# Optimization experiments

Measured on AMD Instinct MI355X. Metric: run time of the kernel, lower is better.

## Reference

```python
import jax, jax.numpy as jnp
import numpy as np

B, T, D_MODEL, D_HEAD = 8, 2048, 1024, 64


def setup_inputs() -> dict:
    key = jax.random.key(0)
    kx, kq, kk, kv = jax.random.split(key, 4)
    s = 1.0 / np.sqrt(D_MODEL)
    return {
        "x": jax.random.normal(kx, (B, T, D_MODEL), dtype=jnp.float32),
        "W_Q": jax.random.normal(kq, (D_MODEL, D_HEAD), dtype=jnp.float32) * s,
        "W_K": jax.random.normal(kk, (D_MODEL, D_HEAD), dtype=jnp.float32) * s,
        "W_V": jax.random.normal(kv, (D_MODEL, D_HEAD), dtype=jnp.float32) * s,
    }


def reference(x, W_Q, W_K, W_V):
    # x: [B, T, d_model]; projections -> [B, T, d_head]
    q = jnp.einsum("btd,dh->bth", x, W_Q)
    k = jnp.einsum("btd,dh->bth", x, W_K)
    v = jnp.einsum("btd,dh->bth", x, W_V)
    d_head = W_Q.shape[-1]
    scale = 1.0 / jnp.sqrt(jnp.asarray(d_head, dtype=x.dtype))
    # scores: [B, T, T], causal mask (lower-triangular kept)
    scores = jnp.einsum("bqh,bkh->bqk", q, k) * scale
    T_ = x.shape[1]
    causal = jnp.tril(jnp.ones((T_, T_), dtype=bool))
    scores = jnp.where(causal[None, :, :], scores, jnp.asarray(-jnp.inf, dtype=x.dtype))
    a = jax.nn.softmax(scores, axis=-1)
    # dropout omitted (eval mode / identity)
    out = jnp.einsum("bqk,bkh->bqh", a, v)
    return out
```

## Files before the change

### kernel.cpp

```cpp
#include <hip/hip_runtime.h>

#define TT   2048
#define DM   1024
#define DH   64
#define NB   8
#define BK   128
#define KST  72

typedef __attribute__((ext_vector_type(4))) float          f32x4;
typedef __attribute__((ext_vector_type(4))) int            i32x4;
typedef __attribute__((ext_vector_type(4))) unsigned short u16x4;
typedef __attribute__((ext_vector_type(8))) short          s16x8;

__device__ __forceinline__ unsigned short f2bf(float f) {
  unsigned int u = __float_as_uint(f);
  u += 0x7fffu + ((u >> 16) & 1u);
  return (unsigned short)(u >> 16);
}

#define MFMA(acc, a, b) \
  (acc) = __builtin_amdgcn_mfma_f32_16x16x32_bf16((a), (b), (acc), 0, 0, 0)

__device__ __forceinline__ void gload_lds16(const void* g, void* l) {
  __builtin_amdgcn_global_load_lds(
      (const __attribute__((address_space(1))) void*)g,
      (__attribute__((address_space(3))) void*)l, 16, 0, 0);
}

#define WS_WT    0u
#define WS_QK    393216u
#define WS_VT    4587520u
#define WS_OP    6684672u
#define WS_ML    24510464u

__global__ __launch_bounds__(256) void pack_w_kernel(
    const float* __restrict__ wq, const float* __restrict__ wk,
    const float* __restrict__ wv, unsigned short* __restrict__ wt) {
  int idx = blockIdx.x * 256 + threadIdx.x;
  if (idx >= 192 * DM) return;
  int n = idx >> 10;
  int k = idx & (DM - 1);
  const float* src = (n < 64) ? wq : ((n < 128) ? wk : wv);
  wt[(size_t)n * DM + k] = f2bf(src[(size_t)k * DH + (n & 63)]);
}

__global__ __launch_bounds__(256) void qkv_gemm_kernel(
    const float* __restrict__ x, const unsigned short* __restrict__ wt,
    unsigned short* __restrict__ qkvqk, unsigned short* __restrict__ vt) {
  __shared__ __align__(16) float          a_lds[32 * BK];
  __shared__ __align__(16) unsigned short b_lds[192 * BK];

  const int tid  = threadIdx.x;
  const int lane = tid & 63;
  const int w    = tid >> 6;
  const int ln   = lane & 15;
  const int quad = lane >> 4;
  const int mw   = w & 1;
  const int nw   = w >> 1;
  const int m0   = blockIdx.x * 32;
  const int n0   = nw * 96;
  const int lsw  = ln & 7;

  int agoff[4];
  #pragma unroll
  for (int i = 0; i < 4; ++i) {
    int s = i * 256 + w * 64 + lane;
    int m = s >> 5, cc = s & 31;
    agoff[i] = (m0 + m) * DM + ((cc ^ (m & 7)) << 2);
  }
  int bgoff[12];
  #pragma unroll
  for (int j = 0; j < 12; ++j) {
    int s = j * 256 + w * 64 + lane;
    int n = s >> 4, cc = s & 15;
    bgoff[j] = n * DM + ((cc ^ (n & 7)) << 3);
  }

  f32x4 acc[6];
  #pragma unroll
  for (int i = 0; i < 6; ++i) acc[i] = (f32x4){0.f, 0.f, 0.f, 0.f};
  union { s16x8 v; unsigned short h[8]; } ap;

  #pragma unroll
  for (int i = 0; i < 4; ++i)
    gload_lds16(x + agoff[i], (void*)(a_lds + (i * 256 + w * 64) * 4));
  #pragma unroll
  for (int j = 0; j < 12; ++j)
    gload_lds16(wt + bgoff[j], (void*)(b_lds + (j * 256 + w * 64) * 8));

  for (int k0 = 0; k0 < DM; k0 += BK) {
    __syncthreads();
    #pragma unroll
    for (int ks = 0; ks < BK; ks += 32) {
      const int m  = mw * 16 + ln;
      const int c0 = (ks >> 2) + 2 * quad;
      f32x4 v0 = *(const f32x4*)&a_lds[m * BK + ((c0 ^ lsw) << 2)];
      f32x4 v1 = *(const f32x4*)&a_lds[m * BK + (((c0 + 1) ^ lsw) << 2)];
      #pragma unroll
      for (int j = 0; j < 4; ++j) { ap.h[j] = f2bf(v0[j]); ap.h[4 + j] = f2bf(v1[j]); }
      s16x8 af = ap.v;
      const int cb = (ks >> 3) + quad;
      #pragma unroll
      for (int nt = 0; nt < 6; ++nt) {
        int n = n0 + nt * 16 + ln;
        s16x8 bf = *(const s16x8*)&b_lds[n * BK + ((cb ^ lsw) << 3)];
        MFMA(acc[nt], af, bf);
      }
    }
    __syncthreads();
    if (k0 + BK < DM) {
      const int kn = k0 + BK;
      #pragma unroll
      for (int i = 0; i < 4; ++i)
        gload_lds16(x + agoff[i] + kn, (void*)(a_lds + (i * 256 + w * 64) * 4));
      #pragma unroll
      for (int j = 0; j < 12; ++j)
        gload_lds16(wt + bgoff[j] + kn, (void*)(b_lds + (j * 256 + w * 64) * 8));
    }
  }

  const float QS = 0.18033688011112042f;
  const int mm0 = m0 + mw * 16;
  const int bz  = mm0 >> 11;
  const int tb  = (mm0 & 2047) + quad * 4;
  #pragma unroll
  for (int nt = 0; nt < 6; ++nt) {
    const int ncol = n0 + nt * 16 + ln;
    if (ncol < 128) {
      const float sc = (ncol < 64) ? QS : 1.0f;
      #pragma unroll
      for (int r = 0; r < 4; ++r) {
        int row = mm0 + quad * 4 + r;
        qkvqk[(size_t)row * 128 + ncol] = f2bf(acc[nt][r] * sc);
      }
    } else {
      int d = ncol - 128;
      u16x4 h;
      #pragma unroll
      for (int r = 0; r < 4; ++r) h[r] = f2bf(acc[nt][r]);
      *(u16x4*)(vt + ((size_t)bz * 64 + d) * TT + tb) = h;
    }
  }
}

__global__ __launch_bounds__(256) void attn_part_kernel(
    const unsigned short* __restrict__ qkvqk, const unsigned short* __restrict__ vt,
    unsigned short* __restrict__ opart, float* __restrict__ ml) {
  const int Ctab[16] = {0,1,3,6,10,15,21,28,36,45,55,66,78,91,105,120};
  const int f  = blockIdx.x;
  const int bz = f / 136;
  const int rw = f - bz * 136;
  int s = 0;
  #pragma unroll
  for (int t = 1; t < 16; ++t) if (rw >= Ctab[t]) s = t;
  const int c = rw - Ctab[s];
  const int qtA = 2 * s, qtB = 2 * s + 1;

  __shared__ __align__(16) unsigned short k_lds[128 * 64];
  __shared__ __align__(16) unsigned short v_lds[64 * 128];
  __shared__ __align__(16) unsigned short p_lds[64 * KST];

  const int tid  = threadIdx.x;
  const int w    = tid >> 6;
  const int lane = tid & 63;
  const int ln   = lane & 15;
  const int quad = lane >> 4;
  const int lsw  = ln & 7;
  const int bb   = bz * TT;
  const int kbase = c * 128;

  #pragma unroll
  for (int i = 0; i < 4; ++i) {
    int base = (i * 4 + w) * 64;
    int slot = base + lane;
    int row = slot >> 3, cc = slot & 7;
    gload_lds16(qkvqk + (size_t)(bb + kbase + row) * 128 + 64 + ((cc ^ (row & 7)) << 3),
                (void*)(k_lds + base * 8));
  }
  #pragma unroll
  for (int i = 0; i < 4; ++i) {
    int base = (i * 4 + w) * 64;
    int slot = base + lane;
    int d = slot >> 4, cc = slot & 15;
    gload_lds16(vt + ((size_t)bz * 64 + d) * TT + kbase + ((cc ^ (d & 7)) << 3),
                (void*)(v_lds + base * 8));
  }

  const unsigned short* qrowA = qkvqk + (size_t)(bb + qtA * 64 + w * 16 + ln) * 128;
  const unsigned short* qrowB = qrowA + 64 * 128;
  const s16x8 qfA0 = *(const s16x8*)(qrowA + quad * 8);
  const s16x8 qfA1 = *(const s16x8*)(qrowA + 32 + quad * 8);
  const s16x8 qfB0 = *(const s16x8*)(qrowB + quad * 8);
  const s16x8 qfB1 = *(const s16x8*)(qrowB + 32 + quad * 8);

  s16x8 ones;
  #pragma unroll
  for (int j = 0; j < 8; ++j) ones[j] = (short)0x3F80;

  f32x4 acc_oA[4], acc_oB[4], acc_lA, acc_lB;
  #pragma unroll
  for (int i = 0; i < 4; ++i) {
    acc_oA[i] = (f32x4){0.f, 0.f, 0.f, 0.f};
    acc_oB[i] = (f32x4){0.f, 0.f, 0.f, 0.f};
  }
  acc_lA = (f32x4){0.f, 0.f, 0.f, 0.f};
  acc_lB = (f32x4){0.f, 0.f, 0.f, 0.f};

  const int qgA = qtA * 64 + w * 16 + quad * 4;
  const int qgB = qgA + 64;
  __syncthreads();

  #pragma unroll
  for (int ct = 0; ct < 2; ++ct) {
    const int ktg = c * 2 + ct;
    const int kc0 = quad;
    const int kc1 = 4 + quad;

    if (ktg <= qtA) {
      const bool diag = (ktg == qtA);
      f32x4 acc_s[4];
      #pragma unroll
      for (int i = 0; i < 4; ++i) acc_s[i] = (f32x4){0.f, 0.f, 0.f, 0.f};
      #pragma unroll
      for (int ns = 0; ns < 4; ++ns) {
        const int krow = ct * 64 + ns * 16 + ln;
        s16x8 kf0 = *(const s16x8*)&k_lds[krow * 64 + ((kc0 ^ lsw) << 3)];
        s16x8 kf1 = *(const s16x8*)&k_lds[krow * 64 + ((kc1 ^ lsw) << 3)];
        MFMA(acc_s[ns], qfA0, kf0);
        MFMA(acc_s[ns], qfA1, kf1);
      }
      #pragma unroll
      for (int r = 0; r < 4; ++r) {
        const int qg = qgA + r;
        #pragma unroll
        for (int ns = 0; ns < 4; ++ns) {
          float sv = acc_s[ns][r];
          if (diag) {
            int kg = ktg * 64 + ns * 16 + ln;
            sv = (kg <= qg) ? sv : -1e30f;
          }
          p_lds[(w * 16 + quad * 4 + r) * KST + ns * 16 + ln] = f2bf(exp2f(sv));
        }
      }
      #pragma unroll
      for (int kk = 0; kk < 64; kk += 32) {
        s16x8 pf = *(const s16x8*)&p_lds[(w * 16 + ln) * KST + kk + quad * 8];
        MFMA(acc_lA, pf, ones);
        #pragma unroll
        for (int nt = 0; nt < 4; ++nt) {
          const int d  = nt * 16 + ln;
          const int sc = (ct * 8 + (kk >> 3) + quad) ^ lsw;
          s16x8 vf = *(const s16x8*)&v_lds[d * 128 + sc * 8];
          MFMA(acc_oA[nt], pf, vf);
        }
      }
      asm volatile("" ::: "memory");
    }

    {
      const bool diag = (ktg == qtB);
      f32x4 acc_s[4];
      #pragma unroll
      for (int i = 0; i < 4; ++i) acc_s[i] = (f32x4){0.f, 0.f, 0.f, 0.f};
      #pragma unroll
      for (int ns = 0; ns < 4; ++ns) {
        const int krow = ct * 64 + ns * 16 + ln;
        s16x8 kf0 = *(const s16x8*)&k_lds[krow * 64 + ((kc0 ^ lsw) << 3)];
        s16x8 kf1 = *(const s16x8*)&k_lds[krow * 64 + ((kc1 ^ lsw) << 3)];
        MFMA(acc_s[ns], qfB0, kf0);
        MFMA(acc_s[ns], qfB1, kf1);
      }
      #pragma unroll
      for (int r = 0; r < 4; ++r) {
        const int qg = qgB + r;
        #pragma unroll
        for (int ns = 0; ns < 4; ++ns) {
          float sv = acc_s[ns][r];
          if (diag) {
            int kg = ktg * 64 + ns * 16 + ln;
            sv = (kg <= qg) ? sv : -1e30f;
          }
          p_lds[(w * 16 + quad * 4 + r) * KST + ns * 16 + ln] = f2bf(exp2f(sv));
        }
      }
      #pragma unroll
      for (int kk = 0; kk < 64; kk += 32) {
        s16x8 pf = *(const s16x8*)&p_lds[(w * 16 + ln) * KST + kk + quad * 8];
        MFMA(acc_lB, pf, ones);
        #pragma unroll
        for (int nt = 0; nt < 4; ++nt) {
          const int d  = nt * 16 + ln;
          const int sc = (ct * 8 + (kk >> 3) + quad) ^ lsw;
          s16x8 vf = *(const s16x8*)&v_lds[d * 128 + sc * 8];
          MFMA(acc_oB[nt], pf, vf);
        }
      }
      asm volatile("" ::: "memory");
    }
  }

  #pragma unroll
  for (int half = 0; half < 2; ++half) {
    const int qt = (half == 0) ? qtA : qtB;
    const int g  = qt >> 1;
    const int base = (qt & 1) ? (g + 1) * (g + 1) : g * (g + 1);
    const size_t slab = (size_t)bz * 272 + base + c;
    unsigned short* op = opart + slab * 4096;
    const f32x4* ao = (half == 0) ? acc_oA : acc_oB;
    const f32x4  al = (half == 0) ? acc_lA : acc_lB;
    #pragma unroll
    for (int nt = 0; nt < 4; ++nt)
      #pragma unroll
      for (int r = 0; r < 4; ++r)
        op[(w * 16 + quad * 4 + r) * 64 + nt * 16 + ln] = f2bf(ao[nt][r]);
    if (ln == 0) {
      float* lp = ml + slab * 64;
      #pragma unroll
      for (int r = 0; r < 4; ++r)
        lp[w * 16 + quad * 4 + r] = al[r];
    }
  }
}

__global__ __launch_bounds__(256) void attn_combine_kernel(
    const unsigned short* __restrict__ opart, const float* __restrict__ ml,
    float* __restrict__ out) {
  const int qt = blockIdx.x;
  const int bz = blockIdx.y;
  const int g  = qt >> 1;
  const int nch = g + 1;
  const int base = (qt & 1) ? (g + 1) * (g + 1) : g * (g + 1);
  const size_t slab0 = (size_t)bz * 272 + base;

  const int tid = threadIdx.x;
  const int row = tid >> 2;
  const int ds  = (tid & 3) * 16;

  float L = 0.f;
  float acc[16];
  #pragma unroll
  for (int j = 0; j < 16; ++j) acc[j] = 0.f;
  #pragma unroll 4
  for (int ch = 0; ch < nch; ++ch) {
    L += ml[(slab0 + ch) * 64 + row];
    const unsigned short* op = opart + (slab0 + ch) * 4096 + row * 64 + ds;
    i32x4 v0 = *(const i32x4*)(op);
    i32x4 v1 = *(const i32x4*)(op + 8);
    #pragma unroll
    for (int j = 0; j < 4; ++j) {
      unsigned int u0 = (unsigned int)v0[j], u1 = (unsigned int)v1[j];
      acc[j * 2]         += __uint_as_float(u0 << 16);
      acc[j * 2 + 1]     += __uint_as_float(u0 & 0xffff0000u);
      acc[8 + j * 2]     += __uint_as_float(u1 << 16);
      acc[8 + j * 2 + 1] += __uint_as_float(u1 & 0xffff0000u);
    }
  }
  float inv = 1.0f / L;
  float* o = out + ((size_t)bz * TT + qt * 64 + row) * 64 + ds;
  #pragma unroll
  for (int j = 0; j < 16; ++j) o[j] = acc[j] * inv;
}

extern "C" void kernel_launch(void* const* d_in, const int* in_sizes, int n_in,
                              void* d_out, int out_size, void* d_ws, size_t ws_size,
                              hipStream_t stream) {
  const float* x  = (const float*)d_in[0];
  const float* wq = (const float*)d_in[1];
  const float* wk = (const float*)d_in[2];
  const float* wv = (const float*)d_in[3];
  float* out = (float*)d_out;

  char* ws = (char*)d_ws;
  unsigned short* wt    = (unsigned short*)(ws + WS_WT);
  unsigned short* qkvqk = (unsigned short*)(ws + WS_QK);
  unsigned short* vt    = (unsigned short*)(ws + WS_VT);
  unsigned short* opart = (unsigned short*)(ws + WS_OP);
  float*          ml    = (float*)(ws + WS_ML);

  pack_w_kernel<<<(192 * DM + 255) / 256, 256, 0, stream>>>(wq, wk, wv, wt);
  qkv_gemm_kernel<<<NB * TT / 32, 256, 0, stream>>>(x, wt, qkvqk, vt);
  attn_part_kernel<<<NB * 136, 256, 0, stream>>>(qkvqk, vt, opart, ml);
  attn_combine_kernel<<<dim3(32, NB), 256, 0, stream>>>(opart, ml, out);
}
```

Before: 135.3 us.

## Split attention partial block into two wave groups, one per query tile

The attention partial kernel now launches 512 threads per block. The two query tiles that previously ran one after the other in each wave are handed to two separate groups of four waves, each with its own P scratch buffer in LDS. The K/V tile loads are spread over the eight waves, and exp2f is replaced by the hardware exp2 builtin. This aims to raise parallelism and shorten the serial chain per wave, at the cost of more LDS per block and possibly lower block occupancy.

```diff
diff --git a/kernel.cpp b/kernel.cpp
--- a/kernel.cpp
+++ b/kernel.cpp
@@ -143,7 +143,7 @@
   }
 }
 
-__global__ __launch_bounds__(256) void attn_part_kernel(
+__global__ __launch_bounds__(512) void attn_part_kernel(
     const unsigned short* __restrict__ qkvqk, const unsigned short* __restrict__ vt,
     unsigned short* __restrict__ opart, float* __restrict__ ml) {
   const int Ctab[16] = {0,1,3,6,10,15,21,28,36,45,55,66,78,91,105,120};
@@ -154,171 +154,116 @@
   #pragma unroll
   for (int t = 1; t < 16; ++t) if (rw >= Ctab[t]) s = t;
   const int c = rw - Ctab[s];
-  const int qtA = 2 * s, qtB = 2 * s + 1;
 
   __shared__ __align__(16) unsigned short k_lds[128 * 64];
   __shared__ __align__(16) unsigned short v_lds[64 * 128];
-  __shared__ __align__(16) unsigned short p_lds[64 * KST];
+  __shared__ __align__(16) unsigned short p_lds[2 * 64 * KST];
 
   const int tid  = threadIdx.x;
   const int w    = tid >> 6;
+  const int grp  = w >> 2;
+  const int wq   = w & 3;
   const int lane = tid & 63;
   const int ln   = lane & 15;
   const int quad = lane >> 4;
   const int lsw  = ln & 7;
   const int bb   = bz * TT;
   const int kbase = c * 128;
-
-  #pragma unroll
-  for (int i = 0; i < 4; ++i) {
-    int base = (i * 4 + w) * 64;
+  const int qt   = 2 * s + grp;
+
+  #pragma unroll
+  for (int i = 0; i < 2; ++i) {
+    int base = i * 512 + w * 64;
     int slot = base + lane;
     int row = slot >> 3, cc = slot & 7;
     gload_lds16(qkvqk + (size_t)(bb + kbase + row) * 128 + 64 + ((cc ^ (row & 7)) << 3),
                 (void*)(k_lds + base * 8));
   }
   #pragma unroll
-  for (int i = 0; i < 4; ++i) {
-    int base = (i * 4 + w) * 64;
+  for (int i = 0; i < 2; ++i) {
+    int base = i * 512 + w * 64;
     int slot = base + lane;
     int d = slot >> 4, cc = slot & 15;
     gload_lds16(vt + ((size_t)bz * 64 + d) * TT + kbase + ((cc ^ (d & 7)) << 3),
                 (void*)(v_lds + base * 8));
   }
 
-  const unsigned short* qrowA = qkvqk + (size_t)(bb + qtA * 64 + w * 16 + ln) * 128;
-  const unsigned short* qrowB = qrowA + 64 * 128;
-  const s16x8 qfA0 = *(const s16x8*)(qrowA + quad * 8);
-  const s16x8 qfA1 = *(const s16x8*)(qrowA + 32 + quad * 8);
-  const s16x8 qfB0 = *(const s16x8*)(qrowB + quad * 8);
-  const s16x8 qfB1 = *(const s16x8*)(qrowB + 32 + quad * 8);
+  const unsigned short* qrow = qkvqk + (size_t)(bb + qt * 64 + wq * 16 + ln) * 128;
+  const s16x8 qf0 = *(const s16x8*)(qrow + quad * 8);
+  const s16x8 qf1 = *(const s16x8*)(qrow + 32 + quad * 8);
 
   s16x8 ones;
   #pragma unroll
   for (int j = 0; j < 8; ++j) ones[j] = (short)0x3F80;
 
-  f32x4 acc_oA[4], acc_oB[4], acc_lA, acc_lB;
-  #pragma unroll
-  for (int i = 0; i < 4; ++i) {
-    acc_oA[i] = (f32x4){0.f, 0.f, 0.f, 0.f};
-    acc_oB[i] = (f32x4){0.f, 0.f, 0.f, 0.f};
-  }
-  acc_lA = (f32x4){0.f, 0.f, 0.f, 0.f};
-  acc_lB = (f32x4){0.f, 0.f, 0.f, 0.f};
-
-  const int qgA = qtA * 64 + w * 16 + quad * 4;
-  const int qgB = qgA + 64;
+  f32x4 acc_o[4], acc_l;
+  #pragma unroll
+  for (int i = 0; i < 4; ++i) acc_o[i] = (f32x4){0.f, 0.f, 0.f, 0.f};
+  acc_l = (f32x4){0.f, 0.f, 0.f, 0.f};
+
+  unsigned short* pb = p_lds + grp * 64 * KST;
+  const int qg = qt * 64 + wq * 16 + quad * 4;
   __syncthreads();
 
   #pragma unroll
   for (int ct = 0; ct < 2; ++ct) {
     const int ktg = c * 2 + ct;
-    const int kc0 = quad;
-    const int kc1 = 4 + quad;
-
-    if (ktg <= qtA) {
-      const bool diag = (ktg == qtA);
+    if (ktg <= qt) {
+      const bool diag = (ktg == qt);
       f32x4 acc_s[4];
       #pragma unroll
       for (int i = 0; i < 4; ++i) acc_s[i] = (f32x4){0.f, 0.f, 0.f, 0.f};
       #pragma unroll
       for (int ns = 0; ns < 4; ++ns) {
         const int krow = ct * 64 + ns * 16 + ln;
-        s16x8 kf0 = *(const s16x8*)&k_lds[krow * 64 + ((kc0 ^ lsw) << 3)];
-        s16x8 kf1 = *(const s16x8*)&k_lds[krow * 64 + ((kc1 ^ lsw) << 3)];
-        MFMA(acc_s[ns], qfA0, kf0);
-        MFMA(acc_s[ns], qfA1, kf1);
+        s16x8 kf0 = *(const s16x8*)&k_lds[krow * 64 + ((quad ^ lsw) << 3)];
+        s16x8 kf1 = *(const s16x8*)&k_lds[krow * 64 + (((4 + quad) ^ lsw) << 3)];
+        MFMA(acc_s[ns], qf0, kf0);
+        MFMA(acc_s[ns], qf1, kf1);
       }
       #pragma unroll
       for (int r = 0; r < 4; ++r) {
-        const int qg = qgA + r;
+        const int qgr = qg + r;
         #pragma unroll
         for (int ns = 0; ns < 4; ++ns) {
           float sv = acc_s[ns][r];
           if (diag) {
             int kg = ktg * 64 + ns * 16 + ln;
-            sv = (kg <= qg) ? sv : -1e30f;
+            sv = (kg <= qgr) ? sv : -1e30f;
           }
-          p_lds[(w * 16 + quad * 4 + r) * KST + ns * 16 + ln] = f2bf(exp2f(sv));
+          pb[(wq * 16 + quad * 4 + r) * KST + ns * 16 + ln] =
+              f2bf(__builtin_amdgcn_exp2f(sv));
         }
       }
       #pragma unroll
       for (int kk = 0; kk < 64; kk += 32) {
-        s16x8 pf = *(const s16x8*)&p_lds[(w * 16 + ln) * KST + kk + quad * 8];
-        MFMA(acc_lA, pf, ones);
+        s16x8 pf = *(const s16x8*)&pb[(wq * 16 + ln) * KST + kk + quad * 8];
+        MFMA(acc_l, pf, ones);
         #pragma unroll
         for (int nt = 0; nt < 4; ++nt) {
           const int d  = nt * 16 + ln;
           const int sc = (ct * 8 + (kk >> 3) + quad) ^ lsw;
           s16x8 vf = *(const s16x8*)&v_lds[d * 128 + sc * 8];
-          MFMA(acc_oA[nt], pf, vf);
+          MFMA(acc_o[nt], pf, vf);
         }
       }
       asm volatile("" ::: "memory");
     }
-
-    {
-      const bool diag = (ktg == qtB);
-      f32x4 acc_s[4];
-      #pragma unroll
-      for (int i = 0; i < 4; ++i) acc_s[i] = (f32x4){0.f, 0.f, 0.f, 0.f};
-      #pragma unroll
-      for (int ns = 0; ns < 4; ++ns) {
-        const int krow = ct * 64 + ns * 16 + ln;
-        s16x8 kf0 = *(const s16x8*)&k_lds[krow * 64 + ((kc0 ^ lsw) << 3)];
-        s16x8 kf1 = *(const s16x8*)&k_lds[krow * 64 + ((kc1 ^ lsw) << 3)];
-        MFMA(acc_s[ns], qfB0, kf0);
-        MFMA(acc_s[ns], qfB1, kf1);
-      }
-      #pragma unroll
-      for (int r = 0; r < 4; ++r) {
-        const int qg = qgB + r;
-        #pragma unroll
-        for (int ns = 0; ns < 4; ++ns) {
-          float sv = acc_s[ns][r];
-          if (diag) {
-            int kg = ktg * 64 + ns * 16 + ln;
-            sv = (kg <= qg) ? sv : -1e30f;
-          }
-          p_lds[(w * 16 + quad * 4 + r) * KST + ns * 16 + ln] = f2bf(exp2f(sv));
-        }
-      }
-      #pragma unroll
-      for (int kk = 0; kk < 64; kk += 32) {
-        s16x8 pf = *(const s16x8*)&p_lds[(w * 16 + ln) * KST + kk + quad * 8];
-        MFMA(acc_lB, pf, ones);
-        #pragma unroll
-        for (int nt = 0; nt < 4; ++nt) {
-          const int d  = nt * 16 + ln;
-          const int sc = (ct * 8 + (kk >> 3) + quad) ^ lsw;
-          s16x8 vf = *(const s16x8*)&v_lds[d * 128 + sc * 8];
-          MFMA(acc_oB[nt], pf, vf);
-        }
-      }
-      asm volatile("" ::: "memory");
-    }
-  }
-
-  #pragma unroll
-  for (int half = 0; half < 2; ++half) {
-    const int qt = (half == 0) ? qtA : qtB;
-    const int g  = qt >> 1;
-    const int base = (qt & 1) ? (g + 1) * (g + 1) : g * (g + 1);
-    const size_t slab = (size_t)bz * 272 + base + c;
-    unsigned short* op = opart + slab * 4096;
-    const f32x4* ao = (half == 0) ? acc_oA : acc_oB;
-    const f32x4  al = (half == 0) ? acc_lA : acc_lB;
+  }
+
+  const int base = (qt & 1) ? (s + 1) * (s + 1) : s * (s + 1);
+  const size_t slab = (size_t)bz * 272 + base + c;
+  unsigned short* op = opart + slab * 4096;
+  #pragma unroll
+  for (int nt = 0; nt < 4; ++nt)
     #pragma unroll
-    for (int nt = 0; nt < 4; ++nt)
-      #pragma unroll
-      for (int r = 0; r < 4; ++r)
-        op[(w * 16 + quad * 4 + r) * 64 + nt * 16 + ln] = f2bf(ao[nt][r]);
-    if (ln == 0) {
-      float* lp = ml + slab * 64;
-      #pragma unroll
-      for (int r = 0; r < 4; ++r)
-        lp[w * 16 + quad * 4 + r] = al[r];
-    }
+    for (int r = 0; r < 4; ++r)
+      op[(wq * 16 + quad * 4 + r) * 64 + nt * 16 + ln] = f2bf(acc_o[nt][r]);
+  if (ln == 0) {
+    float* lp = ml + slab * 64;
+    #pragma unroll
+    for (int r = 0; r < 4; ++r)
+      lp[wq * 16 + quad * 4 + r] = acc_l[r];
   }
 }
 
@@ -379,6 +324,6 @@
 
   pack_w_kernel<<<(192 * DM + 255) / 256, 256, 0, stream>>>(wq, wk, wv, wt);
   qkv_gemm_kernel<<<NB * TT / 32, 256, 0, stream>>>(x, wt, qkvqk, vt);
-  attn_part_kernel<<<NB * 136, 256, 0, stream>>>(qkvqk, vt, opart, ml);
+  attn_part_kernel<<<NB * 136, 512, 0, stream>>>(qkvqk, vt, opart, ml);
   attn_combine_kernel<<<dim3(32, NB), 256, 0, stream>>>(opart, ml, out);
 }
```

New measurement: 132.3 us. -2.3%, faster.
